# Kernel optimization log

Measured on AMD Instinct MI355X. Metric: run time of the kernel, lower is better.

The kernel has to match this reference:

```python
import jax, jax.numpy as jnp
import numpy as np

NUM_SAMPLED_ROIS = 512
FG_FRACTION = 0.25
FG_IOU_THR = 0.5
BG_IOU_HIGH = 0.5
BG_IOU_LOW = 0.0
IMG_SIZE = 1024.0


def _make_boxes(key, shape):
    kc, ks = jax.random.split(key)
    c = jax.random.uniform(kc, shape + (2,)) * IMG_SIZE            # centers (y, x)
    s = jax.random.uniform(ks, shape + (2,)) * 128.0 + 8.0         # sizes
    lo = jnp.clip(c - s * 0.5, 0.0, IMG_SIZE)
    hi = jnp.clip(c + s * 0.5, 0.0, IMG_SIZE)
    return jnp.concatenate([lo, hi], axis=-1)                       # [ymin, xmin, ymax, xmax]


def setup_inputs() -> dict:
    key = jax.random.key(0)
    k1, k2, k3, k4 = jax.random.split(key, 4)
    B, N, M = 32, 8192, 256
    boxes = _make_boxes(k1, (B, N))
    gt_raw = _make_boxes(k2, (B, M))
    num_valid = jax.random.randint(k3, (B,), 8, M + 1)
    valid = jnp.arange(M)[None, :] < num_valid[:, None]            # [B, M]
    gt_boxes = jnp.where(valid[..., None], gt_raw, -jnp.ones_like(gt_raw))
    cls = jax.random.randint(k4, (B, M), 1, 91, dtype=jnp.int32)
    gt_classes = jnp.where(valid, cls, -jnp.ones_like(cls))
    return {"boxes": boxes, "gt_boxes": gt_boxes, "gt_classes": gt_classes}


def _bbox_overlap(boxes, gt_boxes):
    # boxes [B,N,4], gt_boxes [B,M,4] -> IoU [B,N,M]; invalid (padded) gt -> -1
    b = boxes[:, :, None, :]
    g = gt_boxes[:, None, :, :]
    iy0 = jnp.maximum(b[..., 0], g[..., 0])
    ix0 = jnp.maximum(b[..., 1], g[..., 1])
    iy1 = jnp.minimum(b[..., 2], g[..., 2])
    ix1 = jnp.minimum(b[..., 3], g[..., 3])
    inter = jnp.maximum(iy1 - iy0, 0.0) * jnp.maximum(ix1 - ix0, 0.0)
    area_b = (boxes[..., 2] - boxes[..., 0]) * (boxes[..., 3] - boxes[..., 1])
    area_g = (gt_boxes[..., 2] - gt_boxes[..., 0]) * (gt_boxes[..., 3] - gt_boxes[..., 1])
    union = area_b[:, :, None] + area_g[:, None, :] - inter
    iou = jnp.where(union > 0.0, inter / union, 0.0)
    gt_invalid = jnp.max(gt_boxes, axis=-1) < 0.0                  # [B, M]
    return jnp.where(gt_invalid[:, None, :], -1.0, iou)


def _rank_desc(score):
    # rank of each element when sorted by descending score, per row
    order = jnp.argsort(-score, axis=1)
    return jnp.argsort(order, axis=1)


def _sample_indices(key, positive, negative, num_samples, fg_fraction):
    # balanced fg/bg sampling: up to num_fg random positives, fill rest with negatives
    B, Np = positive.shape
    num_fg = int(num_samples * fg_fraction)
    r = jax.random.uniform(key, (B, Np))
    pos_rank = _rank_desc(jnp.where(positive, r, -1.0))
    sel_pos = positive & (pos_rank < num_fg)
    n_pos = jnp.sum(sel_pos, axis=1, keepdims=True)
    neg_rank = _rank_desc(jnp.where(negative, r, -1.0))
    sel_neg = negative & (neg_rank < (num_samples - n_pos))
    selected = sel_pos | sel_neg
    # prefer selected candidates; random tie-break fills any shortfall
    score = selected.astype(jnp.float32) * 2.0 + r
    _, idx = jax.lax.top_k(score, num_samples)
    return idx                                                      # [B, K]


def reference(boxes, gt_boxes, gt_classes):
    gt_boxes = gt_boxes.astype(boxes.dtype)
    boxes = jnp.concatenate([boxes, gt_boxes], axis=1)              # mix gt boxes
    iou = _bbox_overlap(boxes, gt_boxes)                            # [B, N', M]

    matched_vals = jnp.max(iou, axis=-1)                            # [B, N']
    matched_idx = jnp.argmax(iou, axis=-1).astype(jnp.int32)
    indicator = jnp.where(
        matched_vals >= FG_IOU_THR, 1,
        jnp.where(matched_vals >= BG_IOU_HIGH, -2,
                  jnp.where(matched_vals >= BG_IOU_LOW, -1, -3)))

    positive = indicator >= 0
    negative = indicator == -1
    ignored = indicator == -2
    invalid = indicator == -3
    background = negative | invalid                                 # [B, N']

    g_cls = jnp.take_along_axis(gt_classes, matched_idx, axis=1)
    matched_gt_classes = jnp.where(background, 0, g_cls)
    g_box = jnp.take_along_axis(gt_boxes, matched_idx[..., None], axis=1)
    matched_gt_boxes = jnp.where(background[..., None], 0.0, g_box)
    matched_gt_indices = jnp.where(background, -1, matched_idx)

    idx = _sample_indices(jax.random.key(42), positive, negative & ~ignored,
                          NUM_SAMPLED_ROIS, FG_FRACTION)

    sampled_rois = jnp.take_along_axis(boxes, idx[..., None], axis=1)
    sampled_gt_boxes = jnp.take_along_axis(matched_gt_boxes, idx[..., None], axis=1)
    sampled_gt_classes = jnp.take_along_axis(matched_gt_classes, idx, axis=1)
    sampled_gt_indices = jnp.take_along_axis(matched_gt_indices, idx, axis=1)
    return sampled_rois, sampled_gt_boxes, sampled_gt_classes, sampled_gt_indices
```

## Files before the change

kernel.cpp:

```cpp
#include <hip/hip_runtime.h>
#include <stdint.h>

#define BATCH 32
#define NBOX 8192
#define MGT 256
#define NP 8448
#define NUM_SAMP 512
#define NUM_FG 128
#define NBUCK 2048
#define CANDCAP 1024

__device__ __forceinline__ uint32_t rotl32(uint32_t x, uint32_t r) {
  return (x << r) | (x >> (32u - r));
}

__device__ __forceinline__ uint32_t threefry_bits(uint32_t f) {
  uint32_t x0 = 0u;
  uint32_t x1 = f;
  const uint32_t ks0 = 0u, ks1 = 42u;
  const uint32_t ks2 = 0x1BD11BDAu ^ ks0 ^ ks1;
  const uint32_t k[3] = {ks0, ks1, ks2};
  x0 += ks0; x1 += ks1;
  const uint32_t rotA[4] = {13u, 15u, 26u, 6u};
  const uint32_t rotB[4] = {17u, 29u, 16u, 24u};
#pragma unroll
  for (int g = 0; g < 5; ++g) {
#pragma unroll
    for (int q = 0; q < 4; ++q) {
      uint32_t rr = (g & 1) ? rotB[q] : rotA[q];
      x0 += x1; x1 = rotl32(x1, rr); x1 ^= x0;
    }
    x0 += k[(g + 1) % 3];
    x1 += k[(g + 2) % 3] + (uint32_t)(g + 1);
  }
  return x0 ^ x1;
}

__global__ __launch_bounds__(256) void k1_compute(const float* __restrict__ boxes,
                                                  const float* __restrict__ gt_boxes,
                                                  uint32_t* __restrict__ packed,
                                                  int* __restrict__ midx_ws) {
  const int b = blockIdx.y;
  const int i = blockIdx.x * 256 + threadIdx.x;
  __shared__ float4 sg[MGT];
  __shared__ float sga[MGT];
  __shared__ int nv_s;
  if (threadIdx.x == 0) nv_s = MGT;
  __syncthreads();
  {
    const int j = threadIdx.x;
    float4 g = ((const float4*)gt_boxes)[b * MGT + j];
    sg[j] = g;
    sga[j] = __fmul_rn(__fsub_rn(g.z, g.x), __fsub_rn(g.w, g.y));
    if (g.x < 0.0f) atomicMin(&nv_s, j);
  }
  __syncthreads();
  const int nv = nv_s;

  float4 bx;
  if (i < NBOX) bx = ((const float4*)boxes)[b * NBOX + i];
  else          bx = ((const float4*)gt_boxes)[b * MGT + (i - NBOX)];
  const float area_b = __fmul_rn(__fsub_rn(bx.z, bx.x), __fsub_rn(bx.w, bx.y));

  const double CHALF = 0.5 - 0x1p-26;
  float bestq = -1.0f;
  int bestj = -1;
#pragma unroll 4
  for (int j = 0; j < nv; ++j) {
    float4 g = sg[j];
    float iy0 = fmaxf(bx.x, g.x);
    float ix0 = fmaxf(bx.y, g.y);
    float iy1 = fminf(bx.z, g.z);
    float ix1 = fminf(bx.w, g.w);
    float ih = fmaxf(__fsub_rn(iy1, iy0), 0.0f);
    float iw = fmaxf(__fsub_rn(ix1, ix0), 0.0f);
    float inter = __fmul_rn(ih, iw);
    if (inter > 0.0f) {
      float u = __fsub_rn(__fadd_rn(area_b, sga[j]), inter);
      if ((double)inter >= (double)u * CHALF) {
        float q = __fdiv_rn(inter, u);
        if (q > bestq) { bestq = q; bestj = j; }
      }
    }
  }

  const bool pos = (bestj >= 0);
  const uint32_t bits = threefry_bits((uint32_t)(b * NP + i));
  const uint32_t mant = bits >> 9;
  const uint32_t inv = 0x7FFFFFu - mant;
  packed[b * NP + i] = (inv << 1) | (pos ? 1u : 0u);
  midx_ws[b * NP + i] = bestj;
}

__device__ __forceinline__ void emit_lds(unsigned long long* __restrict__ sk,
                                         int* __restrict__ cnt,
                                         uint32_t idx, uint32_t inv) {
  uint32_t mant = 0x7FFFFFu - inv;
  float r = __uint_as_float(0x3F800000u | mant) - 1.0f;
  float score = __fadd_rn(2.0f, r);
  uint32_t sb = __float_as_uint(score);
  unsigned long long key =
      ((unsigned long long)(~sb) << 14) | (unsigned long long)idx;
  int slot = atomicAdd(cnt, 1);
  if (slot < NUM_SAMP) sk[slot] = key;
}

__global__ __launch_bounds__(512) void k23_select_sort_gather(
    const uint32_t* __restrict__ packed, const float* __restrict__ boxes,
    const float* __restrict__ gt_boxes, const int* __restrict__ gt_classes,
    const int* __restrict__ midx_ws, float* __restrict__ out) {
  const int b = blockIdx.x;
  const int tid = threadIdx.x;
  __shared__ uint32_t srow[NP];
  __shared__ uint32_t hist[NBUCK];
  __shared__ uint32_t wsum[8];
  __shared__ unsigned long long cand[2][CANDCAP];
  __shared__ unsigned long long sk[NUM_SAMP];
  __shared__ int candn[2];
  __shared__ int cutb[2], rem[2];
  __shared__ int npos_s, selcnt_s;

  if (tid == 0) { selcnt_s = 0; candn[0] = 0; candn[1] = 0; }
  {
    const uint4* row4 = (const uint4*)(packed + b * NP);
    for (int k = tid; k < NP / 4; k += 512) ((uint4*)srow)[k] = row4[k];
    for (int k = tid; k < NBUCK; k += 512) hist[k] = 0;
    if (tid < NUM_SAMP) sk[tid] = ~0ull;
  }
  __syncthreads();

  for (int idx = tid; idx < NP; idx += 512) {
    uint32_t w = srow[idx];
    atomicAdd(&hist[(w >> 1) >> 12], (w & 1u) ? 0x10000u : 1u);
  }
  __syncthreads();

  const int base = tid * 4;
  uint32_t csum = 0;
#pragma unroll
  for (int q = 0; q < 4; ++q) csum += hist[base + q];
  uint32_t incl = csum;
#pragma unroll
  for (int d = 1; d < 64; d <<= 1) {
    uint32_t v = __shfl_up(incl, d, 64);
    if ((tid & 63) >= d) incl += v;
  }
  const int wid = tid >> 6;
  if ((tid & 63) == 63) wsum[wid] = incl;
  __syncthreads();
  {
    uint32_t prefix = 0;
#pragma unroll
    for (int w = 0; w < 8; ++w) prefix += (w < wid) ? wsum[w] : 0u;
    incl += prefix;
  }
  const uint32_t excl = incl - csum;
  if (tid == 511) {
    const int tpos = (int)(incl >> 16);
    const int tneg = (int)(incl & 0xFFFFu);
    npos_s = tpos;
    if (tpos < NUM_FG) { cutb[1] = NBUCK; rem[1] = 0; }
    const int npc = (tpos < NUM_FG) ? tpos : NUM_FG;
    const int Ln = NUM_SAMP - npc;
    if (Ln == 0)        { cutb[0] = -1;    rem[0] = 0; }
    else if (tneg < Ln) { cutb[0] = NBUCK; rem[0] = 0; }
  }
  __syncthreads();
  {
    const uint32_t L = NUM_FG;
    uint32_t pe = excl >> 16, pi = incl >> 16;
    if (pe < L && pi >= L) {
      uint32_t run = pe;
#pragma unroll
      for (int q = 0; q < 4; ++q) {
        uint32_t h = hist[base + q] >> 16;
        if (run + h >= L) { cutb[1] = base + q; rem[1] = (int)(L - run); break; }
        run += h;
      }
    }
  }
  {
    const int npc = (npos_s < NUM_FG) ? npos_s : NUM_FG;
    const uint32_t L = (uint32_t)(NUM_SAMP - npc);
    uint32_t ne = excl & 0xFFFFu, ni = incl & 0xFFFFu;
    if (L > 0 && ne < L && ni >= L) {
      uint32_t run = ne;
#pragma unroll
      for (int q = 0; q < 4; ++q) {
        uint32_t h = hist[base + q] & 0xFFFFu;
        if (run + h >= L) { cutb[0] = base + q; rem[0] = (int)(L - run); break; }
        run += h;
      }
    }
  }
  __syncthreads();

  for (int idx = tid; idx < NP; idx += 512) {
    uint32_t w = srow[idx];
    uint32_t f = w & 1u;
    uint32_t inv = w >> 1;
    int bk = (int)(inv >> 12);
    if (bk < cutb[f]) {
      emit_lds(sk, &selcnt_s, (uint32_t)idx, inv);
    } else if (bk == cutb[f]) {
      int s = atomicAdd(&candn[f], 1);
      if (s < CANDCAP)
        cand[f][s] = ((unsigned long long)inv << 14) | (unsigned long long)idx;
    }
  }
  __syncthreads();

  for (int f = 0; f < 2; ++f) {
    int n = candn[f]; if (n > CANDCAP) n = CANDCAP;
    for (int c = tid; c < n; c += 512) {
      unsigned long long me = cand[f][c];
      int r = 0;
      for (int j = 0; j < n; ++j) r += (cand[f][j] < me) ? 1 : 0;
      if (r < rem[f])
        emit_lds(sk, &selcnt_s, (uint32_t)(me & 0x3FFFull),
                 (uint32_t)(me >> 14));
    }
  }

  bool prevCross = true;
  for (int k = 2; k <= NUM_SAMP; k <<= 1) {
    for (int j = k >> 1; j > 0; j >>= 1) {
      const bool cross = (j >= 64);
      if (cross || prevCross) __syncthreads();
      else __builtin_amdgcn_wave_barrier();
      const int t = tid, ixj = t ^ j;
      if (ixj > t) {
        unsigned long long a = sk[t], c = sk[ixj];
        bool asc = ((t & k) == 0);
        if ((a > c) == asc) { sk[t] = c; sk[ixj] = a; }
      }
      prevCross = cross;
    }
  }
  __syncthreads();

  const int gtb_base = BATCH * NUM_SAMP * 4;
  const int cls_base = 2 * BATCH * NUM_SAMP * 4;
  const int idx_base = cls_base + BATCH * NUM_SAMP;

  for (int t = tid; t < NUM_SAMP; t += 512) {
    unsigned long long key = sk[t];
    int i = (int)(key & 0x3FFFull);
    if (i >= NP) i = NP - 1;
    float4 roi;
    if (i < NBOX) roi = ((const float4*)boxes)[b * NBOX + i];
    else          roi = ((const float4*)gt_boxes)[b * MGT + (i - NBOX)];
    const int o4 = (b * NUM_SAMP + t) * 4;
    out[o4 + 0] = roi.x;
    out[o4 + 1] = roi.y;
    out[o4 + 2] = roi.z;
    out[o4 + 3] = roi.w;

    const int midx = midx_ws[b * NP + i];
    float4 gb = make_float4(0.0f, 0.0f, 0.0f, 0.0f);
    float cls = 0.0f;
    if (midx >= 0) {
      gb = ((const float4*)gt_boxes)[b * MGT + midx];
      cls = (float)gt_classes[b * MGT + midx];
    }
    out[gtb_base + o4 + 0] = gb.x;
    out[gtb_base + o4 + 1] = gb.y;
    out[gtb_base + o4 + 2] = gb.z;
    out[gtb_base + o4 + 3] = gb.w;
    out[cls_base + b * NUM_SAMP + t] = cls;
    out[idx_base + b * NUM_SAMP + t] = (float)midx;
  }
}

extern "C" void kernel_launch(void* const* d_in, const int* in_sizes, int n_in,
                              void* d_out, int out_size, void* d_ws, size_t ws_size,
                              hipStream_t stream) {
  const float* boxes      = (const float*)d_in[0];
  const float* gt_boxes   = (const float*)d_in[1];
  const int*   gt_classes = (const int*)d_in[2];
  float* out = (float*)d_out;

  char* ws = (char*)d_ws;
  uint32_t* packed = (uint32_t*)(ws);
  int* midx_ws     = (int*)(ws + 1081344);

  k1_compute<<<dim3(NP / 256, BATCH), 256, 0, stream>>>(boxes, gt_boxes, packed,
                                                        midx_ws);
  k23_select_sort_gather<<<BATCH, 512, 0, stream>>>(packed, boxes, gt_boxes,
                                                    gt_classes, midx_ws, out);
}
```

Baseline: 106.6 us.

## Fuse IoU compute and select/sort stages into one cooperative kernel

Merges the IoU/random-key kernel and the per-batch select, sort and gather kernel into one cooperative launch with a grid-wide sync between them. Shared memory for the two phases is overlaid through a union, and the second phase runs on one 256-thread block per batch instead of 512 threads. It also stops staging the packed row in LDS and reads it from global memory twice. This removes a kernel launch boundary but adds a grid barrier, halves the threads in the serial selection phase, and leaves most blocks idle after the sync.

```diff
diff --git a/kernel.cpp b/kernel.cpp
--- a/kernel.cpp
+++ b/kernel.cpp
@@ -1,5 +1,8 @@
 #include <hip/hip_runtime.h>
+#include <hip/hip_cooperative_groups.h>
 #include <stdint.h>
+
+namespace cg = cooperative_groups;
 
 #define BATCH 32
 #define NBOX 8192
@@ -8,7 +11,7 @@
 #define NUM_SAMP 512
 #define NUM_FG 128
 #define NBUCK 2048
-#define CANDCAP 1024
+#define CANDCAP 512
 
 __device__ __forceinline__ uint32_t rotl32(uint32_t x, uint32_t r) {
   return (x << r) | (x >> (32u - r));
@@ -36,61 +39,19 @@
   return x0 ^ x1;
 }
 
-__global__ __launch_bounds__(256) void k1_compute(const float* __restrict__ boxes,
-                                                  const float* __restrict__ gt_boxes,
-                                                  uint32_t* __restrict__ packed,
-                                                  int* __restrict__ midx_ws) {
-  const int b = blockIdx.y;
-  const int i = blockIdx.x * 256 + threadIdx.x;
-  __shared__ float4 sg[MGT];
-  __shared__ float sga[MGT];
-  __shared__ int nv_s;
-  if (threadIdx.x == 0) nv_s = MGT;
-  __syncthreads();
-  {
-    const int j = threadIdx.x;
-    float4 g = ((const float4*)gt_boxes)[b * MGT + j];
-    sg[j] = g;
-    sga[j] = __fmul_rn(__fsub_rn(g.z, g.x), __fsub_rn(g.w, g.y));
-    if (g.x < 0.0f) atomicMin(&nv_s, j);
-  }
-  __syncthreads();
-  const int nv = nv_s;
-
-  float4 bx;
-  if (i < NBOX) bx = ((const float4*)boxes)[b * NBOX + i];
-  else          bx = ((const float4*)gt_boxes)[b * MGT + (i - NBOX)];
-  const float area_b = __fmul_rn(__fsub_rn(bx.z, bx.x), __fsub_rn(bx.w, bx.y));
-
-  const double CHALF = 0.5 - 0x1p-26;
-  float bestq = -1.0f;
-  int bestj = -1;
-#pragma unroll 4
-  for (int j = 0; j < nv; ++j) {
-    float4 g = sg[j];
-    float iy0 = fmaxf(bx.x, g.x);
-    float ix0 = fmaxf(bx.y, g.y);
-    float iy1 = fminf(bx.z, g.z);
-    float ix1 = fminf(bx.w, g.w);
-    float ih = fmaxf(__fsub_rn(iy1, iy0), 0.0f);
-    float iw = fmaxf(__fsub_rn(ix1, ix0), 0.0f);
-    float inter = __fmul_rn(ih, iw);
-    if (inter > 0.0f) {
-      float u = __fsub_rn(__fadd_rn(area_b, sga[j]), inter);
-      if ((double)inter >= (double)u * CHALF) {
-        float q = __fdiv_rn(inter, u);
-        if (q > bestq) { bestq = q; bestj = j; }
-      }
-    }
-  }
-
-  const bool pos = (bestj >= 0);
-  const uint32_t bits = threefry_bits((uint32_t)(b * NP + i));
-  const uint32_t mant = bits >> 9;
-  const uint32_t inv = 0x7FFFFFu - mant;
-  packed[b * NP + i] = (inv << 1) | (pos ? 1u : 0u);
-  midx_ws[b * NP + i] = bestj;
-}
+struct ShA {
+  float4 sg[MGT];
+  float sga[MGT];
+  int nv;
+};
+struct ShB {
+  uint32_t hist[NBUCK];
+  unsigned long long cand[2][CANDCAP];
+  unsigned long long sk[NUM_SAMP];
+  uint32_t wsum[4];
+  int candn[2], cutb[2], rem[2], npos, selcnt;
+};
+union ShU { ShA a; ShB b; };
 
 __device__ __forceinline__ void emit_lds(unsigned long long* __restrict__ sk,
                                          int* __restrict__ cnt,
@@ -105,40 +66,84 @@
   if (slot < NUM_SAMP) sk[slot] = key;
 }
 
-__global__ __launch_bounds__(512) void k23_select_sort_gather(
-    const uint32_t* __restrict__ packed, const float* __restrict__ boxes,
-    const float* __restrict__ gt_boxes, const int* __restrict__ gt_classes,
-    const int* __restrict__ midx_ws, float* __restrict__ out) {
-  const int b = blockIdx.x;
+__global__ __launch_bounds__(256, 5) void fused_roi(
+    const float* __restrict__ boxes, const float* __restrict__ gt_boxes,
+    const int* __restrict__ gt_classes, uint32_t* __restrict__ packed,
+    int* __restrict__ midx_ws, float* __restrict__ out) {
+  __shared__ ShU sh;
   const int tid = threadIdx.x;
-  __shared__ uint32_t srow[NP];
-  __shared__ uint32_t hist[NBUCK];
-  __shared__ uint32_t wsum[8];
-  __shared__ unsigned long long cand[2][CANDCAP];
-  __shared__ unsigned long long sk[NUM_SAMP];
-  __shared__ int candn[2];
-  __shared__ int cutb[2], rem[2];
-  __shared__ int npos_s, selcnt_s;
-
-  if (tid == 0) { selcnt_s = 0; candn[0] = 0; candn[1] = 0; }
+
   {
-    const uint4* row4 = (const uint4*)(packed + b * NP);
-    for (int k = tid; k < NP / 4; k += 512) ((uint4*)srow)[k] = row4[k];
-    for (int k = tid; k < NBUCK; k += 512) hist[k] = 0;
-    if (tid < NUM_SAMP) sk[tid] = ~0ull;
-  }
-  __syncthreads();
-
-  for (int idx = tid; idx < NP; idx += 512) {
-    uint32_t w = srow[idx];
-    atomicAdd(&hist[(w >> 1) >> 12], (w & 1u) ? 0x10000u : 1u);
-  }
-  __syncthreads();
-
-  const int base = tid * 4;
+    const int b = blockIdx.y;
+    const int i = blockIdx.x * 256 + tid;
+    if (tid == 0) sh.a.nv = MGT;
+    __syncthreads();
+    {
+      float4 g = ((const float4*)gt_boxes)[b * MGT + tid];
+      sh.a.sg[tid] = g;
+      sh.a.sga[tid] = __fmul_rn(__fsub_rn(g.z, g.x), __fsub_rn(g.w, g.y));
+      if (g.x < 0.0f) atomicMin(&sh.a.nv, tid);
+    }
+    __syncthreads();
+    const int nv = sh.a.nv;
+
+    float4 bx;
+    if (i < NBOX) bx = ((const float4*)boxes)[b * NBOX + i];
+    else          bx = ((const float4*)gt_boxes)[b * MGT + (i - NBOX)];
+    const float area_b = __fmul_rn(__fsub_rn(bx.z, bx.x), __fsub_rn(bx.w, bx.y));
+
+    const double CHALF = 0.5 - 0x1p-26;
+    float bestq = -1.0f;
+    int bestj = -1;
+#pragma unroll 4
+    for (int j = 0; j < nv; ++j) {
+      float4 g = sh.a.sg[j];
+      float iy0 = fmaxf(bx.x, g.x);
+      float ix0 = fmaxf(bx.y, g.y);
+      float iy1 = fminf(bx.z, g.z);
+      float ix1 = fminf(bx.w, g.w);
+      float ih = fmaxf(__fsub_rn(iy1, iy0), 0.0f);
+      float iw = fmaxf(__fsub_rn(ix1, ix0), 0.0f);
+      float inter = __fmul_rn(ih, iw);
+      if (inter > 0.0f) {
+        float u = __fsub_rn(__fadd_rn(area_b, sh.a.sga[j]), inter);
+        if ((double)inter >= (double)u * CHALF) {
+          float q = __fdiv_rn(inter, u);
+          if (q > bestq) { bestq = q; bestj = j; }
+        }
+      }
+    }
+
+    const bool pos = (bestj >= 0);
+    const uint32_t bits = threefry_bits((uint32_t)(b * NP + i));
+    const uint32_t mant = bits >> 9;
+    const uint32_t inv = 0x7FFFFFu - mant;
+    packed[b * NP + i] = (inv << 1) | (pos ? 1u : 0u);
+    midx_ws[b * NP + i] = bestj;
+  }
+
+  cg::this_grid().sync();
+  if (blockIdx.x != 0) return;
+
+  const int b = blockIdx.y;
+  const uint32_t* __restrict__ rowp = packed + b * NP;
+
+  if (tid == 0) { sh.b.selcnt = 0; sh.b.candn[0] = 0; sh.b.candn[1] = 0; }
+  for (int k = tid; k < NBUCK; k += 256) sh.b.hist[k] = 0;
+  sh.b.sk[tid] = ~0ull;
+  sh.b.sk[tid + 256] = ~0ull;
+  __syncthreads();
+
+  for (int idx = tid; idx < NP; idx += 256) {
+    uint32_t w = rowp[idx];
+    atomicAdd(&sh.b.hist[(w >> 1) >> 12], (w & 1u) ? 0x10000u : 1u);
+  }
+  __syncthreads();
+
+  const int base = tid * 8;
   uint32_t csum = 0;
 #pragma unroll
-  for (int q = 0; q < 4; ++q) csum += hist[base + q];
+  for (int q = 0; q < 8; ++q) csum += sh.b.hist[base + q];
   uint32_t incl = csum;
 #pragma unroll
   for (int d = 1; d < 64; d <<= 1) {
@@ -146,24 +151,24 @@
     if ((tid & 63) >= d) incl += v;
   }
   const int wid = tid >> 6;
-  if ((tid & 63) == 63) wsum[wid] = incl;
+  if ((tid & 63) == 63) sh.b.wsum[wid] = incl;
   __syncthreads();
   {
     uint32_t prefix = 0;
 #pragma unroll
-    for (int w = 0; w < 8; ++w) prefix += (w < wid) ? wsum[w] : 0u;
+    for (int w = 0; w < 4; ++w) prefix += (w < wid) ? sh.b.wsum[w] : 0u;
     incl += prefix;
   }
   const uint32_t excl = incl - csum;
-  if (tid == 511) {
+  if (tid == 255) {
     const int tpos = (int)(incl >> 16);
     const int tneg = (int)(incl & 0xFFFFu);
-    npos_s = tpos;
-    if (tpos < NUM_FG) { cutb[1] = NBUCK; rem[1] = 0; }
+    sh.b.npos = tpos;
+    if (tpos < NUM_FG) { sh.b.cutb[1] = NBUCK; sh.b.rem[1] = 0; }
     const int npc = (tpos < NUM_FG) ? tpos : NUM_FG;
     const int Ln = NUM_SAMP - npc;
-    if (Ln == 0)        { cutb[0] = -1;    rem[0] = 0; }
-    else if (tneg < Ln) { cutb[0] = NBUCK; rem[0] = 0; }
+    if (Ln == 0)        { sh.b.cutb[0] = -1;    sh.b.rem[0] = 0; }
+    else if (tneg < Ln) { sh.b.cutb[0] = NBUCK; sh.b.rem[0] = 0; }
   }
   __syncthreads();
   {
@@ -172,52 +177,53 @@
     if (pe < L && pi >= L) {
       uint32_t run = pe;
 #pragma unroll
-      for (int q = 0; q < 4; ++q) {
-        uint32_t h = hist[base + q] >> 16;
-        if (run + h >= L) { cutb[1] = base + q; rem[1] = (int)(L - run); break; }
+      for (int q = 0; q < 8; ++q) {
+        uint32_t h = sh.b.hist[base + q] >> 16;
+        if (run + h >= L) { sh.b.cutb[1] = base + q; sh.b.rem[1] = (int)(L - run); break; }
         run += h;
       }
     }
   }
   {
-    const int npc = (npos_s < NUM_FG) ? npos_s : NUM_FG;
+    const int npc = (sh.b.npos < NUM_FG) ? sh.b.npos : NUM_FG;
     const uint32_t L = (uint32_t)(NUM_SAMP - npc);
     uint32_t ne = excl & 0xFFFFu, ni = incl & 0xFFFFu;
     if (L > 0 && ne < L && ni >= L) {
       uint32_t run = ne;
 #pragma unroll
-      for (int q = 0; q < 4; ++q) {
-        uint32_t h = hist[base + q] & 0xFFFFu;
-        if (run + h >= L) { cutb[0] = base + q; rem[0] = (int)(L - run); break; }
+      for (int q = 0; q < 8; ++q) {
+        uint32_t h = sh.b.hist[base + q] & 0xFFFFu;
+        if (run + h >= L) { sh.b.cutb[0] = base + q; sh.b.rem[0] = (int)(L - run); break; }
         run += h;
       }
     }
   }
   __syncthreads();
 
-  for (int idx = tid; idx < NP; idx += 512) {
-    uint32_t w = srow[idx];
+  for (int idx = tid; idx < NP; idx += 256) {
+    uint32_t w = rowp[idx];
     uint32_t f = w & 1u;
     uint32_t inv = w >> 1;
     int bk = (int)(inv >> 12);
-    if (bk < cutb[f]) {
-      emit_lds(sk, &selcnt_s, (uint32_t)idx, inv);
-    } else if (bk == cutb[f]) {
-      int s = atomicAdd(&candn[f], 1);
+    if (bk < sh.b.cutb[f]) {
+      emit_lds(sh.b.sk, &sh.b.selcnt, (uint32_t)idx, inv);
+    } else if (bk == sh.b.cutb[f]) {
+      int s = atomicAdd(&sh.b.candn[f], 1);
       if (s < CANDCAP)
-        cand[f][s] = ((unsigned long long)inv << 14) | (unsigned long long)idx;
+        sh.b.cand[f][s] =
+            ((unsigned long long)inv << 14) | (unsigned long long)idx;
     }
   }
   __syncthreads();
 
   for (int f = 0; f < 2; ++f) {
-    int n = candn[f]; if (n > CANDCAP) n = CANDCAP;
-    for (int c = tid; c < n; c += 512) {
-      unsigned long long me = cand[f][c];
+    int n = sh.b.candn[f]; if (n > CANDCAP) n = CANDCAP;
+    for (int c = tid; c < n; c += 256) {
+      unsigned long long me = sh.b.cand[f][c];
       int r = 0;
-      for (int j = 0; j < n; ++j) r += (cand[f][j] < me) ? 1 : 0;
-      if (r < rem[f])
-        emit_lds(sk, &selcnt_s, (uint32_t)(me & 0x3FFFull),
+      for (int j = 0; j < n; ++j) r += (sh.b.cand[f][j] < me) ? 1 : 0;
+      if (r < sh.b.rem[f])
+        emit_lds(sh.b.sk, &sh.b.selcnt, (uint32_t)(me & 0x3FFFull),
                  (uint32_t)(me >> 14));
     }
   }
@@ -228,11 +234,14 @@
       const bool cross = (j >= 64);
       if (cross || prevCross) __syncthreads();
       else __builtin_amdgcn_wave_barrier();
-      const int t = tid, ixj = t ^ j;
-      if (ixj > t) {
-        unsigned long long a = sk[t], c = sk[ixj];
-        bool asc = ((t & k) == 0);
-        if ((a > c) == asc) { sk[t] = c; sk[ixj] = a; }
+#pragma unroll
+      for (int p = 0; p < 2; ++p) {
+        const int t = tid + p * 256, ixj = t ^ j;
+        if (ixj > t) {
+          unsigned long long a = sh.b.sk[t], c = sh.b.sk[ixj];
+          bool asc = ((t & k) == 0);
+          if ((a > c) == asc) { sh.b.sk[t] = c; sh.b.sk[ixj] = a; }
+        }
       }
       prevCross = cross;
     }
@@ -243,8 +252,8 @@
   const int cls_base = 2 * BATCH * NUM_SAMP * 4;
   const int idx_base = cls_base + BATCH * NUM_SAMP;
 
-  for (int t = tid; t < NUM_SAMP; t += 512) {
-    unsigned long long key = sk[t];
+  for (int t = tid; t < NUM_SAMP; t += 256) {
+    unsigned long long key = sh.b.sk[t];
     int i = (int)(key & 0x3FFFull);
     if (i >= NP) i = NP - 1;
     float4 roi;
@@ -284,8 +293,8 @@
   uint32_t* packed = (uint32_t*)(ws);
   int* midx_ws     = (int*)(ws + 1081344);
 
-  k1_compute<<<dim3(NP / 256, BATCH), 256, 0, stream>>>(boxes, gt_boxes, packed,
-                                                        midx_ws);
-  k23_select_sort_gather<<<BATCH, 512, 0, stream>>>(packed, boxes, gt_boxes,
-                                                    gt_classes, midx_ws, out);
-}
+  void* args[] = {(void*)&boxes, (void*)&gt_boxes, (void*)&gt_classes,
+                  (void*)&packed, (void*)&midx_ws, (void*)&out};
+  hipLaunchCooperativeKernel((const void*)fused_roi, dim3(NP / 256, BATCH),
+                             dim3(256), args, 0, stream);
+}
```

After: 196.7 us. +84.6%, slower.
